# Performance work log

Hardware: AMD Instinct MI355X
Metric: run time of the kernel (lower is better)

The kernel has to match this reference:

```python
import jax, jax.numpy as jnp
import numpy as np

TOPK = 3
RAT_S = 0.05


def conv4d(x, w, bs):
    """Faithful fused version of the looped Conv4d (stride=1, padding=1, l_k=3).

    x:  (b, c_in, l, d, h, w)
    w:  (c_out, c_in, l_k, d_k, h_k, w_k)  -- w[:, :, i] is the i-th Conv3d weight
    bs: (l_k, c_out)                        -- per-i Conv3d biases
    The torch loop computes out[f] = sum_i conv3d_i(x[f + i - l_k//2]) for valid
    frame indices, which is exactly a 4D cross-correlation; the bias of conv3d_i
    is added once per VALID i, so boundary frames get fewer bias terms.
    """
    out = jax.lax.conv_general_dilated(
        x, w, window_strides=(1, 1, 1, 1), padding=[(1, 1)] * 4,
        dimension_numbers=("NCABXY", "OIABXY", "NCABXY"))
    l_i = x.shape[2]
    l_k = w.shape[2]
    f = jnp.arange(l_i)
    j = f[:, None] + jnp.arange(l_k)[None, :] - l_k // 2  # source frame per (f, i)
    valid = ((j >= 0) & (j < l_i)).astype(x.dtype)        # (l, l_k)
    bias = valid @ bs                                     # (l, c_out)
    return out + bias.T[None, :, :, None, None, None]


def zero_window(x_aff, h, w, rat_s):
    """x_aff: (b, h*w, h, w). Suppress a Gaussian window centered at each
    channel's (r, c) source location."""
    dt = x_aff.dtype
    sr = jnp.asarray(h * rat_s, dt)
    sc = jnp.asarray(w * rat_s, dt)
    ind_r = jnp.arange(h, dtype=dt)
    ind_c = jnp.arange(w, dtype=dt)
    cent_r = jnp.repeat(jnp.arange(h), w).astype(dt)  # (h*w,)
    cent_c = jnp.tile(jnp.arange(w), h).astype(dt)    # (h*w,)
    gr = jnp.exp(-((ind_r[None, :] - cent_r[:, None]) ** 2) / (2 * sr ** 2))  # (hw, h)
    gc = jnp.exp(-((ind_c[None, :] - cent_c[:, None]) ** 2) / (2 * sc ** 2))  # (hw, w)
    g = 1.0 - gr[:, :, None] * gc[:, None, :]  # (hw, h, w)
    return x_aff * g[None]


def setup_inputs() -> dict:
    key = jax.random.key(0)
    k = jax.random.split(key, 5)
    b, c, h, w = 4, 256, 32, 32
    x = jax.random.normal(k[0], (b, c, h, w), dtype=jnp.float32)
    w1 = jax.random.normal(k[1], (16, 1, 3, 3, 3, 3), dtype=jnp.float32) * 0.2
    b1 = jax.random.normal(k[2], (3, 16), dtype=jnp.float32) * 0.05
    w2 = jax.random.normal(k[3], (1, 16, 3, 3, 3, 3), dtype=jnp.float32) * 0.1
    b2 = jax.random.normal(k[4], (3, 1), dtype=jnp.float32) * 0.05
    return {"x": x, "w1": w1, "b1": b1, "w2": w2, "b2": b2}


def reference(x, w1, b1, w2, b2):
    b, c, h1, ww1 = x.shape
    n = h1 * ww1
    # F.normalize over channel dim (p=2, eps=1e-12)
    xn = x / jnp.maximum(jnp.linalg.norm(x, axis=1, keepdims=True), 1e-12)
    q = xn.transpose(0, 2, 3, 1).reshape(b, n, c)      # (b, hw, c)
    kmat = xn.reshape(b, c, n)                          # (b, c, hw)
    aff = jnp.einsum("bnc,bcm->bnm", q, kmat)          # (b, hw, hw)
    aff = zero_window(aff.reshape(b, n, h1, ww1), h1, ww1, RAT_S)
    x_fc = aff.reshape(b, 1, h1, ww1, h1, ww1)
    y = conv4d(x_fc, w1, b1)                            # (b, 16, h1, w1, h2, w2)
    y = conv4d(y, w2, b2)                               # (b, 1,  h1, w1, h2, w2)
    xc = y.reshape(b, n, h1, ww1)                       # (b, hw, h2, w2)
    # top-k values along dim=-3 (the query/channel axis)
    vals = jax.lax.top_k(xc.transpose(0, 2, 3, 1), TOPK)[0]  # (b, h2, w2, k)
    return vals.transpose(0, 3, 1, 2)                   # (b, k, h2, w2)
```

## Files before the change

kernel.cpp:

```cpp
#include <hip/hip_runtime.h>

#define HW 1024
#define CCH 256


typedef _Float16 h2v __attribute__((ext_vector_type(2)));
typedef _Float16 f16x8 __attribute__((ext_vector_type(8)));
typedef short bf16x8 __attribute__((ext_vector_type(8)));
typedef float f32x4 __attribute__((ext_vector_type(4)));

__device__ __forceinline__ float fdot2(unsigned a, unsigned b, float c) {
#if __has_builtin(__builtin_amdgcn_fdot2)
    return __builtin_amdgcn_fdot2(__builtin_bit_cast(h2v, a),
                                  __builtin_bit_cast(h2v, b), c, false);
#else
    h2v ha = __builtin_bit_cast(h2v, a), hb = __builtin_bit_cast(h2v, b);
    return c + (float)ha.x * (float)hb.x + (float)ha.y * (float)hb.y;
#endif
}
__device__ __forceinline__ unsigned packh2(float x, float y) {
    h2v h;
    h.x = (_Float16)x;
    h.y = (_Float16)y;
    return __builtin_bit_cast(unsigned, h);
}
__device__ __forceinline__ unsigned short f2bf(float f) {
    unsigned u = __float_as_uint(f);
    u += 0x7fffu + ((u >> 16) & 1u);
    return (unsigned short)(u >> 16);
}
__device__ __forceinline__ unsigned short f2h(float f) {
    return __builtin_bit_cast(unsigned short, (_Float16)f);
}
__device__ __forceinline__ float h2f(unsigned short u) {
    return (float)__builtin_bit_cast(_Float16, u);
}

__global__ __launch_bounds__(256) void norm_kernel(const float* __restrict__ x,
                                                   unsigned short* __restrict__ xnT) {
    __shared__ float red[16][17];
    __shared__ float invs[16];
    int b = blockIdx.y;
    int p0 = blockIdx.x * 16;
    int cg = threadIdx.x >> 4;
    int pp = threadIdx.x & 15;
    int p = p0 + pp;
    const float* xb = x + (size_t)b * CCH * HW;
    float ss = 0.f;
#pragma unroll
    for (int i = 0; i < 16; ++i) {
        float v = xb[(size_t)(cg * 16 + i) * HW + p];
        ss += v * v;
    }
    red[cg][pp] = ss;
    __syncthreads();
    if (threadIdx.x < 16) {
        float s = 0.f;
#pragma unroll
        for (int g = 0; g < 16; ++g) s += red[g][threadIdx.x];
        invs[threadIdx.x] = 1.0f / fmaxf(sqrtf(s), 1e-12f);
    }
    __syncthreads();
    float inv = invs[pp];
    unsigned* o = (unsigned*)(xnT + ((size_t)b * HW + p) * CCH) + cg * 8;
#pragma unroll
    for (int i = 0; i < 8; ++i) {
        int c = cg * 16 + 2 * i;
        unsigned lo = f2bf(xb[(size_t)c * HW + p] * inv);
        unsigned hi = f2bf(xb[(size_t)(c + 1) * HW + p] * inv);
        o[i] = lo | (hi << 16);
    }
}

__global__ __launch_bounds__(256) void aff_kernel(const unsigned short* __restrict__ xnT,
                                                  unsigned short* __restrict__ Af16) {
    int b = blockIdx.z;
    int p0 = blockIdx.y * 64, m0 = blockIdx.x * 64;
    const unsigned short* X = xnT + (size_t)b * HW * CCH;
    int lane = threadIdx.x & 63, w = threadIdx.x >> 6;
    int pw = p0 + (w >> 1) * 32, mw = m0 + (w & 1) * 32;
    int lr = lane & 15, lg = lane >> 4;
    f32x4 acc[2][2] = {};
    for (int ks = 0; ks < 8; ++ks) {
        int kc = ks * 32 + lg * 8;
        bf16x8 a0 = *(const bf16x8*)&X[(size_t)(pw + lr) * CCH + kc];
        bf16x8 a1 = *(const bf16x8*)&X[(size_t)(pw + 16 + lr) * CCH + kc];
        bf16x8 b0 = *(const bf16x8*)&X[(size_t)(mw + lr) * CCH + kc];
        bf16x8 b1 = *(const bf16x8*)&X[(size_t)(mw + 16 + lr) * CCH + kc];
        acc[0][0] = __builtin_amdgcn_mfma_f32_16x16x32_bf16(a0, b0, acc[0][0], 0, 0, 0);
        acc[0][1] = __builtin_amdgcn_mfma_f32_16x16x32_bf16(a0, b1, acc[0][1], 0, 0, 0);
        acc[1][0] = __builtin_amdgcn_mfma_f32_16x16x32_bf16(a1, b0, acc[1][0], 0, 0, 0);
        acc[1][1] = __builtin_amdgcn_mfma_f32_16x16x32_bf16(a1, b1, acc[1][1], 0, 0, 0);
    }
#pragma unroll
    for (int pi = 0; pi < 2; ++pi)
#pragma unroll
        for (int mi = 0; mi < 2; ++mi)
#pragma unroll
            for (int r = 0; r < 4; ++r) {
                int p = pw + 16 * pi + lg * 4 + r;
                int m = mw + 16 * mi + lr;
                int dr = (m >> 5) - (p >> 5);
                int dc = (m & 31) - (p & 31);
                float gg = 1.0f - __expf(-(float)(dr * dr + dc * dc) * 0.1953125f);
                float v = acc[pi][mi][r] * gg;
                Af16[((size_t)b * HW + p) * HW + m] =
                    __builtin_bit_cast(unsigned short, (_Float16)v);
            }
}

__global__ __launch_bounds__(256) void g_kernel(const float* __restrict__ w1,
                                                const float* __restrict__ w2,
                                                float* __restrict__ G) {
    __shared__ float w1s[1296], w2s[1296];
    int tid = threadIdx.x;
    for (int i = tid; i < 1296; i += 256) { w1s[i] = w1[i]; w2s[i] = w2[i]; }
    __syncthreads();
    int idx = blockIdx.x * 256 + tid;
    if (idx < 6561) {
        int o1 = idx / 81, o2 = idx - o1 * 81;
        float s = 0.f;
#pragma unroll
        for (int ch = 0; ch < 16; ++ch) s += w1s[ch * 81 + o1] * w2s[ch * 81 + o2];
        G[idx] = s;
    }
}

__global__ __launch_bounds__(128) void wcomp_kernel(const float* __restrict__ G,
                                                    unsigned* __restrict__ Wpk,
                                                    unsigned short* __restrict__ Wmf) {
    __shared__ float Gs[6561];
    int cls = blockIdx.x;
    int t = threadIdx.x;
    for (int i = t; i < 6561; i += 128) Gs[i] = G[i];
    if (t < 25) Wpk[cls * 400 + t * 16 + 15] = 0u;
    bool emit = (cls % 9) == 4;
    unsigned short* wm = Wmf + (size_t)(cls / 9) * 1024;
    if (emit) {
        for (int i = t; i < 1024; i += 128) {
            int m = i >> 5, k = i & 31;
            if (m >= 25 || k >= 25) wm[i] = 0;
        }
    }
    __syncthreads();
    if (t >= 125) return;
    int a = t / 25, b_ = (t / 5) % 5, c = t % 5;
    int r1c = cls / 27, c1c = (cls / 9) % 3, r2c = (cls / 3) % 3, c2c = cls % 3;
    float W[5] = {};
    for (int i2 = 0; i2 < 3; ++i2) {
        if ((r1c == 0 && i2 == 0) || (r1c == 2 && i2 == 2)) continue;
        int i1 = a - i2;
        if (i1 < 0 || i1 > 2) continue;
        for (int j2 = 0; j2 < 3; ++j2) {
            if ((c1c == 0 && j2 == 0) || (c1c == 2 && j2 == 2)) continue;
            int j1 = b_ - j2;
            if (j1 < 0 || j1 > 2) continue;
            for (int u2 = 0; u2 < 3; ++u2) {
                if ((r2c == 0 && u2 == 0) || (r2c == 2 && u2 == 2)) continue;
                int u1 = c - u2;
                if (u1 < 0 || u1 > 2) continue;
                for (int v2 = 0; v2 < 3; ++v2) {
                    if ((c2c == 0 && v2 == 0) || (c2c == 2 && v2 == 2)) continue;
                    int o2 = i2 * 27 + j2 * 9 + u2 * 3 + v2;
                    int o1b = i1 * 27 + j1 * 9 + u1 * 3;
#pragma unroll
                    for (int d = 0; d < 5; ++d) {
                        int v1 = d - v2;
                        if (v1 < 0 || v1 > 2) continue;
                        W[d] += Gs[(o1b + v1) * 81 + o2];
                    }
                }
            }
        }
    }
    unsigned* o = &Wpk[cls * 400 + (a * 5 + b_) * 16 + c * 3];
    o[0] = packh2(W[0], W[1]);
    o[1] = packh2(W[2], W[3]);
    o[2] = packh2(W[4], 0.f);
    if (emit) {
        int k = a * 5 + b_;
#pragma unroll
        for (int d = 0; d < 5; ++d) wm[(c * 5 + d) * 32 + k] = f2h(W[d]);
    }
}

__global__ __launch_bounds__(1024) void bt_kernel(const float* __restrict__ w2,
                                                  const float* __restrict__ b1,
                                                  const float* __restrict__ b2,
                                                  float* __restrict__ BT) {
    __shared__ float w2s[1296], b1s[48], S0[81], S1[81], S2[81];
    int t = threadIdx.x;
    for (int i = t; i < 1296; i += 1024) w2s[i] = w2[i];
    if (t < 48) b1s[t] = b1[t];
    __syncthreads();
    if (t < 81) {
        float s0 = 0.f, s1 = 0.f, s2 = 0.f;
#pragma unroll
        for (int ch = 0; ch < 16; ++ch) {
            float w = w2s[ch * 81 + t];
            s0 += w * b1s[16 + ch];
            s1 += w * b1s[ch];
            s2 += w * b1s[32 + ch];
        }
        S0[t] = s0; S1[t] = s1; S2[t] = s2;
    }
    __syncthreads();
    if (t >= 864) return;
    int r1 = t / 27, c1c = (t / 9) % 3, r2c = (t / 3) % 3, c2c = t % 3;
    float s = b2[1] + (r1 >= 1 ? b2[0] : 0.f) + (r1 <= 30 ? b2[2] : 0.f);
    for (int i2 = 0; i2 < 3; ++i2) {
        int rr = r1 + i2 - 1;
        if (rr < 0 || rr > 31) continue;
        float m1 = (rr >= 1) ? 1.f : 0.f, m2 = (rr <= 30) ? 1.f : 0.f;
        for (int j2 = 0; j2 < 3; ++j2) {
            if ((c1c == 0 && j2 == 0) || (c1c == 2 && j2 == 2)) continue;
            for (int u2 = 0; u2 < 3; ++u2) {
                if ((r2c == 0 && u2 == 0) || (r2c == 2 && u2 == 2)) continue;
                for (int v2 = 0; v2 < 3; ++v2) {
                    if ((c2c == 0 && v2 == 0) || (c2c == 2 && v2 == 2)) continue;
                    int o2 = i2 * 27 + j2 * 9 + u2 * 3 + v2;
                    s += S0[o2] + m1 * S1[o2] + m2 * S2[o2];
                }
            }
        }
    }
    BT[t] = s;
}

__global__ __launch_bounds__(256) void convc_kernel(const unsigned short* __restrict__ Af16,
                                                    const unsigned short* __restrict__ Wmf,
                                                    const float* __restrict__ BT,
                                                    float* __restrict__ xc) {
    __shared__ __align__(16) unsigned short S[32768];
    int tid = threadIdx.x;
    int w = tid >> 6, lane = tid & 63;
    int P = blockIdx.x, b = blockIdx.y;
    int r1 = P >> 5, c1 = P & 31;
    int r1c = (r1 == 0) ? 0 : (r1 == 31) ? 2 : 1;
    int c1c = (c1 == 0) ? 0 : (c1 == 31) ? 2 : 1;
    int cls9 = r1c * 3 + c1c;
    float bias = BT[r1 * 27 + c1c * 9 + 4];

    {
        uint4* S4 = (uint4*)S;
        for (int i = tid; i < 4096; i += 256) S4[i] = make_uint4(0, 0, 0, 0);
    }
    __syncthreads();

    for (int i = tid; i < 25 * 128; i += 256) {
        int dp = i >> 7, chunk = i & 127;
        int tr = dp / 5, tc = dp - tr * 5;
        int pr = r1 + tr - 2, pc = c1 + tc - 2;
        if (((unsigned)pr < 32u) && ((unsigned)pc < 32u)) {
            uint4 v = *(const uint4*)&Af16[((size_t)b * HW + pr * 32 + pc) * HW + chunk * 8];
            int kg = dp >> 3;
            int qx = (chunk * 8) ^ (kg << 4);
            *(uint4*)&S[dp * 1024 + qx] = v;
        }
    }

    const unsigned short* wm = Wmf + (size_t)cls9 * 1024;
    int lr = lane & 15, kg2 = lane >> 4;
    f16x8 a0 = *(const f16x8*)&wm[lr * 32 + kg2 * 8];
    f16x8 a1 = *(const f16x8*)&wm[(16 + lr) * 32 + kg2 * 8];

    __syncthreads();

    f32x4 acc0[16], acc1[16];
    int xsh = kg2 << 4;
#pragma unroll
    for (int nt = 0; nt < 16; ++nt) {
        int q = w * 256 + nt * 16 + lr;
        int qq = q ^ xsh;
        const unsigned short* col = &S[kg2 * 8 * 1024 + qq];
        f16x8 bf;
#pragma unroll
        for (int j = 0; j < 8; ++j)
            bf[j] = __builtin_bit_cast(_Float16, col[j * 1024]);
        f32x4 z = {0.f, 0.f, 0.f, 0.f};
        acc0[nt] = __builtin_amdgcn_mfma_f32_16x16x32_f16(a0, bf, z, 0, 0, 0);
        acc1[nt] = __builtin_amdgcn_mfma_f32_16x16x32_f16(a1, bf, z, 0, 0, 0);
    }

    __syncthreads();

#pragma unroll
    for (int nt = 0; nt < 16; ++nt) {
        int q = w * 256 + nt * 16 + lr;
        int tb = kg2 * 4;
#pragma unroll
        for (int r = 0; r < 4; ++r) {
            S[(tb + r) * 1040 + q] = f2h(acc0[nt][r]);
            int t1 = 16 + tb + r;
            if (t1 < 25) S[t1 * 1040 + q] = f2h(acc1[nt][r]);
        }
    }
    __syncthreads();

    float* xp = &xc[((size_t)b * HW + P) * HW];
#pragma unroll
    for (int k = 0; k < 4; ++k) {
        int q = tid + 256 * k;
        int qr = q >> 5, qc = q & 31;
        float s = bias;
#pragma unroll
        for (int u = 0; u < 5; ++u) {
            int rr = qr + u - 2;
            bool rv = ((unsigned)rr < 32u);
            int rbase = rr * 32;
#pragma unroll
            for (int v = 0; v < 5; ++v) {
                int cc = qc + v - 2;
                bool ok = rv && ((unsigned)cc < 32u);
                int idx = ok ? ((u * 5 + v) * 1040 + rbase + cc) : 0;
                float val = h2f(S[idx]);
                s += ok ? val : 0.f;
            }
        }
        xp[q] = s;
    }
}

__global__ __launch_bounds__(256) void expand_kernel(const unsigned short* __restrict__ Af16,
                                                     unsigned* __restrict__ Apad32) {
    int plane = blockIdx.x, b = blockIdx.y;
    const unsigned* src = (const unsigned*)(Af16 + ((size_t)b * HW + plane) * HW);
    unsigned* dst = Apad32 + ((size_t)b * HW + plane) * 720;
    for (int k = threadIdx.x; k < 720; k += 256) {
        int pr = k / 20, pcd = k - pr * 20;
        unsigned val = 0;
        if (pr >= 2 && pr < 34 && pcd >= 1 && pcd <= 16)
            val = src[(pr - 2) * 16 + (pcd - 1)];
        dst[k] = val;
    }
}

__global__ __launch_bounds__(128) void fix_kernel(const unsigned* __restrict__ Apad32,
                                                  const unsigned* __restrict__ Wpk,
                                                  const float* __restrict__ BT,
                                                  float* __restrict__ xc) {
    __shared__ __align__(16) unsigned wl[3600];
    __shared__ float bts[9];
    int tid = threadIdx.x;
    int P = blockIdx.x, b = blockIdx.y;
    int r1 = P >> 5, c1 = P & 31;
    int r1c = (r1 == 0) ? 0 : (r1 == 31) ? 2 : 1;
    int c1c = (c1 == 0) ? 0 : (c1 == 31) ? 2 : 1;

    const unsigned* wsrc = Wpk + (size_t)(r1c * 3 + c1c) * 3600;
    for (int i = tid; i < 3600; i += 128) wl[i] = wsrc[i];
    if (tid < 9) bts[tid] = BT[r1 * 27 + c1c * 9 + tid];

    int li = tid;
    bool act = li < 124;
    int qr, qc;
    if (li < 32) { qr = 0; qc = li; }
    else if (li < 64) { qr = 31; qc = li - 32; }
    else if (li < 94) { qr = li - 63; qc = 0; }
    else { qr = min(li, 123) - 93; qc = 31; }
    int r2c = (qr == 0) ? 0 : (qr == 31) ? 2 : 1;
    int c2c = (qc == 0) ? 0 : (qc == 31) ? 2 : 1;
    int v = r2c * 3 + c2c;
    int sh = (qc & 1) * 16;
    int sd = qc >> 1;

    __syncthreads();
    float acc = 0.f;

#pragma unroll 1
    for (int tp = 0; tp < 25; ++tp) {
        int tr = tp / 5, tc = tp - tr * 5;
        int apr = r1 + tr - 2, apc = c1 + tc - 2;
        if ((unsigned)apr >= 32u || (unsigned)apc >= 32u) continue;
        const unsigned* tpl = Apad32 + ((size_t)b * HW + apr * 32 + apc) * 720;
        const uint4* wv4 = (const uint4*)&wl[v * 400 + tp * 16];
        uint4 wa = wv4[0], wb = wv4[1], wc2 = wv4[2], wd = wv4[3];
        unsigned wr[16] = {wa.x, wa.y, wa.z, wa.w, wb.x, wb.y, wb.z, wb.w,
                           wc2.x, wc2.y, wc2.z, wc2.w, wd.x, wd.y, wd.z, wd.w};
#pragma unroll
        for (int u = 0; u < 5; ++u) {
            const unsigned* rp = tpl + (qr + u) * 20 + sd;
            unsigned d0 = rp[0], d1 = rp[1], d2 = rp[2];
            unsigned pa = __builtin_amdgcn_alignbit(d1, d0, sh);
            unsigned pb = __builtin_amdgcn_alignbit(d2, d1, sh);
            unsigned pc_ = __builtin_amdgcn_alignbit(0u, d2, sh);
            acc = fdot2(wr[u * 3 + 0], pa, acc);
            acc = fdot2(wr[u * 3 + 1], pb, acc);
            acc = fdot2(wr[u * 3 + 2], pc_, acc);
        }
    }

    if (act)
        xc[((size_t)b * HW + P) * HW + qr * 32 + qc] = acc + bts[v];
}

__device__ __forceinline__ void top3_push(float v, float& t0, float& t1, float& t2) {
    float n0 = fminf(t0, v);
    t0 = fmaxf(t0, v);
    float n1 = fminf(t1, n0);
    t1 = fmaxf(t1, n0);
    t2 = fmaxf(t2, n1);
}

__global__ __launch_bounds__(256) void topk1_kernel(const float* __restrict__ xc,
                                                    float* __restrict__ part) {
    int q = blockIdx.x * 256 + threadIdx.x;
    int pc = blockIdx.y, bi = blockIdx.z;
    float t0 = -1e30f, t1 = -1e30f, t2 = -1e30f;
    const float* xp = xc + (size_t)bi * HW * HW;
    for (int p = pc * 32; p < pc * 32 + 32; ++p)
        top3_push(xp[(size_t)p * HW + q], t0, t1, t2);
    float* pp = part + (size_t)(bi * 32 + pc) * 3 * HW;
    pp[q] = t0;
    pp[HW + q] = t1;
    pp[2 * HW + q] = t2;
}

__global__ __launch_bounds__(256) void topk2_kernel(const float* __restrict__ part,
                                                    float* __restrict__ out) {
    int q = blockIdx.x * 256 + threadIdx.x;
    int bi = blockIdx.y;
    float t0 = -1e30f, t1 = -1e30f, t2 = -1e30f;
    const float* pp = part + (size_t)bi * 96 * HW;
    for (int k = 0; k < 96; ++k) top3_push(pp[(size_t)k * HW + q], t0, t1, t2);
    float* ob = out + (size_t)bi * 3 * HW;
    ob[q] = t0;
    ob[HW + q] = t1;
    ob[2 * HW + q] = t2;
}

extern "C" void kernel_launch(void* const* d_in, const int* in_sizes, int n_in,
                              void* d_out, int out_size, void* d_ws, size_t ws_size,
                              hipStream_t stream) {
    const float* x = (const float*)d_in[0];
    const float* w1 = (const float*)d_in[1];
    const float* b1 = (const float*)d_in[2];
    const float* w2 = (const float*)d_in[3];
    const float* b2 = (const float*)d_in[4];
    float* out = (float*)d_out;
    float* ws = (float*)d_ws;

    unsigned short* xnT = (unsigned short*)ws;
    unsigned short* Af16 = (unsigned short*)(ws + 524288);
    float* xc = ws + 2621440;
    unsigned* Wpk = (unsigned*)(ws + 6815744);
    float* BT = ws + 6848512;
    float* part = ws + 6849536;
    unsigned* Apad32 = (unsigned*)(ws + 7242752);
    float* G = ws + 10191872;
    unsigned short* Wmf = (unsigned short*)(ws + 10198440);

    norm_kernel<<<dim3(64, 4), 256, 0, stream>>>(x, xnT);
    aff_kernel<<<dim3(16, 16, 4), 256, 0, stream>>>(xnT, Af16);
    expand_kernel<<<dim3(1024, 4), 256, 0, stream>>>(Af16, Apad32);
    g_kernel<<<26, 256, 0, stream>>>(w1, w2, G);
    wcomp_kernel<<<81, 128, 0, stream>>>(G, Wpk, Wmf);
    bt_kernel<<<1, 1024, 0, stream>>>(w2, b1, b2, BT);
    convc_kernel<<<dim3(1024, 4), 256, 0, stream>>>(Af16, Wmf, BT, xc);
    fix_kernel<<<dim3(1024, 4), 128, 0, stream>>>(Apad32, Wpk, BT, xc);
    topk1_kernel<<<dim3(4, 32, 4), 256, 0, stream>>>(xc, part);
    topk2_kernel<<<dim3(4, 4), 256, 0, stream>>>(part, out);
}
```

Measured before the change: 191.8 us.

## Split convc kernel over query-row bands to cut shared memory and raise occupancy

The convc kernel is split into four row bands per position (grid z-dim added). Each block now loads only 12 query rows (8 plus a 2-row halo on each side) of the 25 neighbour planes into a much smaller shared buffer instead of all 1024 columns. The block runs 6 MFMA tiles per wave instead of 16 and writes 8 output rows. Smaller LDS and register use should allow more resident blocks. The halo rows are loaded redundantly, and the smaller padded strides may change LDS bank conflicts.

```diff
diff --git a/kernel.cpp b/kernel.cpp
--- a/kernel.cpp
+++ b/kernel.cpp
@@ -227,98 +227,108 @@
     BT[t] = s;
 }
 
+#define BST 390
+#define OST 404
 __global__ __launch_bounds__(256) void convc_kernel(const unsigned short* __restrict__ Af16,
                                                     const unsigned short* __restrict__ Wmf,
                                                     const float* __restrict__ BT,
                                                     float* __restrict__ xc) {
-    __shared__ __align__(16) unsigned short S[32768];
+    __shared__ __align__(16) unsigned short S[12480];
     int tid = threadIdx.x;
     int w = tid >> 6, lane = tid & 63;
-    int P = blockIdx.x, b = blockIdx.y;
+    int lr = lane & 15, kg2 = lane >> 4;
+    int P = blockIdx.x, h = blockIdx.y, b = blockIdx.z;
     int r1 = P >> 5, c1 = P & 31;
     int r1c = (r1 == 0) ? 0 : (r1 == 31) ? 2 : 1;
     int c1c = (c1 == 0) ? 0 : (c1 == 31) ? 2 : 1;
     int cls9 = r1c * 3 + c1c;
     float bias = BT[r1 * 27 + c1c * 9 + 4];
-
-    {
-        uint4* S4 = (uint4*)S;
-        for (int i = tid; i < 4096; i += 256) S4[i] = make_uint4(0, 0, 0, 0);
-    }
-    __syncthreads();
-
-    for (int i = tid; i < 25 * 128; i += 256) {
-        int dp = i >> 7, chunk = i & 127;
-        int tr = dp / 5, tc = dp - tr * 5;
-        int pr = r1 + tr - 2, pc = c1 + tc - 2;
-        if (((unsigned)pr < 32u) && ((unsigned)pc < 32u)) {
-            uint4 v = *(const uint4*)&Af16[((size_t)b * HW + pr * 32 + pc) * HW + chunk * 8];
-            int kg = dp >> 3;
-            int qx = (chunk * 8) ^ (kg << 4);
-            *(uint4*)&S[dp * 1024 + qx] = v;
-        }
-    }
+    int qbase = h * 8 - 2;
+
+#pragma unroll 1
+    for (int dp = 0; dp < 32; ++dp) {
+        bool need0 = (dp >= 25);
+        if (!need0) {
+            int pr = r1 + dp / 5 - 2, pc = c1 + dp % 5 - 2;
+            need0 = ((unsigned)pr >= 32u) || ((unsigned)pc >= 32u);
+        }
+        if (need0)
+            for (int i = tid; i < 384; i += 256) S[dp * BST + i] = 0;
+    }
+    __syncthreads();
+
+#pragma unroll 1
+    for (int it = tid; it < 1200; it += 256) {
+        int dp = it % 25, rest = it / 25;
+        int gl = rest >> 2, ch = rest & 3;
+        int g = qbase + gl;
+        int pr = r1 + dp / 5 - 2, pc = c1 + dp % 5 - 2;
+        if (((unsigned)g < 32u) && ((unsigned)pr < 32u) && ((unsigned)pc < 32u)) {
+            uint4 v = *(const uint4*)&Af16[((size_t)b * HW + pr * 32 + pc) * HW + g * 32 + ch * 8];
+            unsigned short* d = &S[dp * BST + gl * 32 + ch * 8];
+            *(unsigned*)(d + 0) = v.x;
+            *(unsigned*)(d + 2) = v.y;
+            *(unsigned*)(d + 4) = v.z;
+            *(unsigned*)(d + 6) = v.w;
+        }
+    }
+    __syncthreads();
 
     const unsigned short* wm = Wmf + (size_t)cls9 * 1024;
-    int lr = lane & 15, kg2 = lane >> 4;
     f16x8 a0 = *(const f16x8*)&wm[lr * 32 + kg2 * 8];
     f16x8 a1 = *(const f16x8*)&wm[(16 + lr) * 32 + kg2 * 8];
 
-    __syncthreads();
-
-    f32x4 acc0[16], acc1[16];
-    int xsh = kg2 << 4;
-#pragma unroll
-    for (int nt = 0; nt < 16; ++nt) {
-        int q = w * 256 + nt * 16 + lr;
-        int qq = q ^ xsh;
-        const unsigned short* col = &S[kg2 * 8 * 1024 + qq];
-        f16x8 bf;
-#pragma unroll
-        for (int j = 0; j < 8; ++j)
-            bf[j] = __builtin_bit_cast(_Float16, col[j * 1024]);
+    f16x8 bf[6];
+#pragma unroll
+    for (int i = 0; i < 6; ++i) {
+        int ql = (w * 6 + i) * 16 + lr;
+        const unsigned short* base = &S[kg2 * 8 * BST + ql];
+        f16x8 t;
+#pragma unroll
+        for (int j = 0; j < 8; ++j) t[j] = __builtin_bit_cast(_Float16, base[j * BST]);
+        bf[i] = t;
+    }
+    __syncthreads();
+
+    f32x4 ac0[6], ac1[6];
+#pragma unroll
+    for (int i = 0; i < 6; ++i) {
         f32x4 z = {0.f, 0.f, 0.f, 0.f};
-        acc0[nt] = __builtin_amdgcn_mfma_f32_16x16x32_f16(a0, bf, z, 0, 0, 0);
-        acc1[nt] = __builtin_amdgcn_mfma_f32_16x16x32_f16(a1, bf, z, 0, 0, 0);
-    }
-
-    __syncthreads();
-
-#pragma unroll
-    for (int nt = 0; nt < 16; ++nt) {
-        int q = w * 256 + nt * 16 + lr;
+        ac0[i] = __builtin_amdgcn_mfma_f32_16x16x32_f16(a0, bf[i], z, 0, 0, 0);
+        ac1[i] = __builtin_amdgcn_mfma_f32_16x16x32_f16(a1, bf[i], z, 0, 0, 0);
+    }
+
+#pragma unroll
+    for (int i = 0; i < 6; ++i) {
+        int ql = (w * 6 + i) * 16 + lr;
         int tb = kg2 * 4;
 #pragma unroll
         for (int r = 0; r < 4; ++r) {
-            S[(tb + r) * 1040 + q] = f2h(acc0[nt][r]);
+            S[(tb + r) * OST + ql] = f2h(ac0[i][r]);
             int t1 = 16 + tb + r;
-            if (t1 < 25) S[t1 * 1040 + q] = f2h(acc1[nt][r]);
-        }
-    }
-    __syncthreads();
-
-    float* xp = &xc[((size_t)b * HW + P) * HW];
-#pragma unroll
-    for (int k = 0; k < 4; ++k) {
-        int q = tid + 256 * k;
-        int qr = q >> 5, qc = q & 31;
-        float s = bias;
-#pragma unroll
-        for (int u = 0; u < 5; ++u) {
-            int rr = qr + u - 2;
-            bool rv = ((unsigned)rr < 32u);
-            int rbase = rr * 32;
-#pragma unroll
-            for (int v = 0; v < 5; ++v) {
-                int cc = qc + v - 2;
-                bool ok = rv && ((unsigned)cc < 32u);
-                int idx = ok ? ((u * 5 + v) * 1040 + rbase + cc) : 0;
-                float val = h2f(S[idx]);
-                s += ok ? val : 0.f;
-            }
-        }
-        xp[q] = s;
-    }
+            if (t1 < 25) S[t1 * OST + ql] = f2h(ac1[i][r]);
+        }
+    }
+    __syncthreads();
+
+    int qrl = tid >> 5, qc = tid & 31;
+    int qr = h * 8 + qrl;
+    float s = bias;
+#pragma unroll
+    for (int u = 0; u < 5; ++u) {
+        int g2 = qr + u - 2;
+        bool rv = ((unsigned)g2 < 32u);
+        int l = qrl + u;
+#pragma unroll
+        for (int v = 0; v < 5; ++v) {
+            int cc = qc + v - 2;
+            bool ok = rv && ((unsigned)cc < 32u);
+            int idx = ok ? ((u * 5 + v) * OST + l * 32 + cc) : 0;
+            float val = h2f(S[idx]);
+            s += ok ? val : 0.f;
+        }
+    }
+    xc[((size_t)b * HW + P) * HW + qr * 32 + qc] = s;
 }
 
 __global__ __launch_bounds__(256) void expand_kernel(const unsigned short* __restrict__ Af16,
@@ -456,7 +466,7 @@
     g_kernel<<<26, 256, 0, stream>>>(w1, w2, G);
     wcomp_kernel<<<81, 128, 0, stream>>>(G, Wpk, Wmf);
     bt_kernel<<<1, 1024, 0, stream>>>(w2, b1, b2, BT);
-    convc_kernel<<<dim3(1024, 4), 256, 0, stream>>>(Af16, Wmf, BT, xc);
+    convc_kernel<<<dim3(1024, 4, 4), 256, 0, stream>>>(Af16, Wmf, BT, xc);
     fix_kernel<<<dim3(1024, 4), 128, 0, stream>>>(Apad32, Wpk, BT, xc);
     topk1_kernel<<<dim3(4, 32, 4), 256, 0, stream>>>(xc, part);
     topk2_kernel<<<dim3(4, 4), 256, 0, stream>>>(part, out);
```

New measurement: 232.4 us. +21.2%, slower.
